# Kernel optimization log

Measured on AMD Instinct MI355X. Metric: run time of the kernel, lower is better.

The kernel has to match this reference:

```python
import jax, jax.numpy as jnp
import numpy as np

B, S, D, H = 2, 2048, 1024, 16
DK = D // H

def setup_inputs() -> dict:
    key = jax.random.key(0)
    ks = jax.random.split(key, 5)
    scale = 1.0 / np.sqrt(D)
    return {
        "query": jax.random.normal(ks[0], (B, S, D), dtype=jnp.float32),
        "mask": jnp.ones((B, S, S), dtype=jnp.int32),
        "Wq": jax.random.normal(ks[1], (D, D), dtype=jnp.float32) * scale,
        "bq": jnp.zeros((D,), dtype=jnp.float32),
        "Wk": jax.random.normal(ks[2], (D, D), dtype=jnp.float32) * scale,
        "bk": jnp.zeros((D,), dtype=jnp.float32),
        "Wv": jax.random.normal(ks[3], (D, D), dtype=jnp.float32) * scale,
        "bv": jnp.zeros((D,), dtype=jnp.float32),
        "Wo": jax.random.normal(ks[4], (D, D), dtype=jnp.float32) * scale,
        "bo": jnp.zeros((D,), dtype=jnp.float32),
    }

def reference(query, mask, Wq, bq, Wk, bk, Wv, bv, Wo, bo):
    # self-attention: key = value = query (torch Linear: x @ W.T + b)
    b, s, d = query.shape
    def proj(x, W, bias):
        y = jnp.einsum('bsd,ed->bse', x, W) + bias
        return y.reshape(b, s, H, DK).transpose(0, 2, 1, 3)  # [B,H,S,DK]
    q = proj(query, Wq, bq)
    k = proj(query, Wk, bk)
    v = proj(query, Wv, bv)
    scores = jnp.einsum('bhqd,bhkd->bhqk', q, k) / jnp.sqrt(jnp.float32(DK))
    m = mask[:, None, :, :]  # [B,1,S,S] (torch unsqueeze(1) for 3D mask)
    scores = jnp.where(m == 0, jnp.float32(-1e9), scores)
    w = jax.nn.softmax(scores, axis=-1)  # dropout: eval mode -> identity
    o = jnp.einsum('bhqk,bhkd->bhqd', w, v)
    o = o.transpose(0, 2, 1, 3).reshape(b, s, d)
    return jnp.einsum('bsd,ed->bse', o, Wo) + bo
```

## Files before the change

### kernel.cpp

```cpp
#include <hip/hip_runtime.h>


typedef _Float16 f16x8 __attribute__((ext_vector_type(8)));
typedef _Float16 f16x4 __attribute__((ext_vector_type(4)));
typedef _Float16 f16x2 __attribute__((ext_vector_type(2)));
typedef float    f32x4 __attribute__((ext_vector_type(4)));
typedef float    f32x16 __attribute__((ext_vector_type(16)));
typedef int      i32x4 __attribute__((ext_vector_type(4)));
typedef unsigned u32x2 __attribute__((ext_vector_type(2)));

#define MFMA32(a, b, c) __builtin_amdgcn_mfma_f32_32x32x16_f16(a, b, c, 0, 0, 0)
#define MFMA16(a, b, c) __builtin_amdgcn_mfma_f32_16x16x32_f16(a, b, c, 0, 0, 0)

#if __has_builtin(__builtin_amdgcn_exp2f)
#define EXP2(x) __builtin_amdgcn_exp2f(x)
#else
#define EXP2(x) exp2f(x)
#endif

__device__ __forceinline__ void gld16(const void* g, void* l) {
    __builtin_amdgcn_global_load_lds(
        (const __attribute__((address_space(1))) void*)g,
        (__attribute__((address_space(3))) void*)l, 16, 0, 0);
}

__device__ __forceinline__ void conv1k(const float* __restrict__ in,
                                       _Float16* __restrict__ out, int base) {
    const int i = base + threadIdx.x * 4;
    float4 v = *(const float4*)(in + i);
    f16x4 o;
    o.x = (_Float16)v.x; o.y = (_Float16)v.y; o.z = (_Float16)v.z; o.w = (_Float16)v.w;
    *(f16x4*)(out + i) = o;
}

__global__ void k_pre(const float* __restrict__ X, const float* __restrict__ Wq,
                      const float* __restrict__ Wk, const float* __restrict__ Wv,
                      const float* __restrict__ Wo,
                      _Float16* __restrict__ Xh, _Float16* __restrict__ Wqh,
                      _Float16* __restrict__ Wkh, _Float16* __restrict__ Wvh,
                      _Float16* __restrict__ Woh,
                      const int* __restrict__ mask, int* __restrict__ flag) {
    const int bid = blockIdx.x;
    if (bid < 4096)      conv1k(X,  Xh,  bid * 1024);
    else if (bid < 5120) conv1k(Wq, Wqh, (bid - 4096) * 1024);
    else if (bid < 6144) conv1k(Wk, Wkh, (bid - 5120) * 1024);
    else if (bid < 7168) conv1k(Wv, Wvh, (bid - 6144) * 1024);
    else if (bid < 8192) conv1k(Wo, Woh, (bid - 7168) * 1024);
    else {
        const int i = (bid - 8192) * 1024 + threadIdx.x * 4;
        int4 v = *(const int4*)(mask + i);
        if ((v.x == 0) | (v.y == 0) | (v.z == 0) | (v.w == 0)) atomicOr(flag, 1);
    }
}

__global__ __launch_bounds__(256, 3) void k_qkv(
    const _Float16* __restrict__ X,
    const _Float16* __restrict__ Wqh, const _Float16* __restrict__ Wkh,
    const _Float16* __restrict__ Wvh,
    const float* __restrict__ bq, const float* __restrict__ bk,
    const float* __restrict__ bv,
    _Float16* __restrict__ Qo, _Float16* __restrict__ Ko, _Float16* __restrict__ Vo)
{
    __shared__ _Float16 SH[128 * 136];
    _Float16* As = SH;
    _Float16* Bs = SH + 128 * 64;
    const int tid = threadIdx.x;
    const int lane = tid & 63, wv = tid >> 6;
    const int wrow = wv >> 1, wcol = wv & 1;
    const int l5 = lane & 31, half = lane >> 5;
    const int which = blockIdx.x >> 3;
    const _Float16* W   = which == 0 ? Wqh : which == 1 ? Wkh : Wvh;
    const float*   bias = which == 0 ? bq  : which == 1 ? bk  : bv;
    const int n0 = (blockIdx.x & 7) * 128;
    const int m0 = blockIdx.y * 128;

    f32x16 acc[2][2];
#pragma unroll
    for (int a = 0; a < 2; ++a)
#pragma unroll
        for (int bb = 0; bb < 2; ++bb)
#pragma unroll
            for (int r = 0; r < 16; ++r) acc[a][bb][r] = 0.f;

#pragma unroll 1
    for (int k0 = 0; k0 < 1024; k0 += 64) {
        __syncthreads();
#pragma unroll
        for (int it = 0; it < 4; ++it) {
            const int wbase = it * 256 + wv * 64;
            const int ci = wbase + lane;
            const int r = ci >> 3;
            const int c8 = (((ci & 7) ^ (r & 7)) * 8);
            gld16(X + (size_t)(m0 + r) * 1024 + k0 + c8, As + wbase * 8);
            gld16(W + (size_t)(n0 + r) * 1024 + k0 + c8, Bs + wbase * 8);
        }
        __syncthreads();
#pragma unroll
        for (int ks = 0; ks < 4; ++ks) {
            f16x8 af[2], bf[2];
#pragma unroll
            for (int mt = 0; mt < 2; ++mt)
                af[mt] = *(const f16x8*)(As + (wrow * 64 + mt * 32 + l5) * 64 +
                                         (((ks * 2 + half) ^ (l5 & 7)) * 8));
#pragma unroll
            for (int nt = 0; nt < 2; ++nt)
                bf[nt] = *(const f16x8*)(Bs + (wcol * 64 + nt * 32 + l5) * 64 +
                                         (((ks * 2 + half) ^ (l5 & 7)) * 8));
#pragma unroll
            for (int mt = 0; mt < 2; ++mt)
#pragma unroll
                for (int nt = 0; nt < 2; ++nt)
                    acc[mt][nt] = MFMA32(af[mt], bf[nt], acc[mt][nt]);
        }
    }

    __syncthreads();
    const int b_ = m0 >> 11;
    const int s_base = m0 & 2047;
    if (which == 2) {
#pragma unroll
        for (int nt = 0; nt < 2; ++nt) {
            const int e_l = wcol * 64 + nt * 32 + l5;
            const float bv_ = bias[n0 + e_l];
#pragma unroll
            for (int mt = 0; mt < 2; ++mt)
#pragma unroll
                for (int g = 0; g < 4; ++g) {
                    const int m_l = wrow * 64 + mt * 32 + 8 * g + 4 * half;
                    f16x4 pk;
#pragma unroll
                    for (int j = 0; j < 4; ++j)
                        pk[j] = (_Float16)(acc[mt][nt][4 * g + j] + bv_);
                    *(f16x4*)(SH + e_l * 136 + m_l) = pk;
                }
        }
        __syncthreads();
#pragma unroll
        for (int p = 0; p < 8; ++p) {
            const int e_l = p * 16 + (tid >> 4);
            const int s8 = (tid & 15) * 8;
            f16x8 vv = *(const f16x8*)(SH + e_l * 136 + s8);
            const int e = n0 + e_l;
            const int h = e >> 6, dk = e & 63;
            const int s0 = s_base + s8;
            const size_t idx = ((((size_t)(b_ * 16 + h) * 128 + (s0 >> 4)) * 2 +
                                (dk >> 5)) * 64 + (dk & 31) + 32 * ((s8 >> 3) & 1)) * 8;
            *(f16x8*)(Vo + idx) = vv;
        }
    } else {
        const float qs = (which == 0) ? 0.18033688011112042f : 1.0f;
#pragma unroll
        for (int nt = 0; nt < 2; ++nt) {
            const int e_l = wcol * 64 + nt * 32 + l5;
            const float bv_ = bias[n0 + e_l];
#pragma unroll
            for (int mt = 0; mt < 2; ++mt)
#pragma unroll
                for (int r = 0; r < 16; ++r) {
                    const int m_l = wrow * 64 + mt * 32 + (r & 3) + 8 * (r >> 2) + 4 * half;
                    SH[m_l * 136 + e_l] = (_Float16)((acc[mt][nt][r] + bv_) * qs);
                }
        }
        __syncthreads();
#pragma unroll
        for (int p = 0; p < 8; ++p) {
            const int m_l = p * 16 + (tid >> 4);
            const int c8 = (tid & 15) * 8;
            f16x8 vv = *(const f16x8*)(SH + m_l * 136 + c8);
            const int e = n0 + c8;
            const int h = e >> 6, dk = e & 63;
            const int s = s_base + m_l;
            if (which == 0) {
                *(f16x8*)(Qo + (((size_t)b_ * 16 + h) * 2048 + s) * 64 + dk) = vv;
            } else {
                const size_t idx = ((((size_t)(b_ * 16 + h) * 64 + (s >> 5)) * 4 +
                                    (dk >> 4)) * 64 + (s & 31) + 32 * ((dk >> 3) & 1)) * 8;
                *(f16x8*)(Ko + idx) = vv;
            }
        }
    }
}

__global__ __launch_bounds__(256, 4) void k_oproj(
    const _Float16* __restrict__ Oin, const _Float16* __restrict__ Woh,
    const float* __restrict__ bo, float* __restrict__ out)
{
    __shared__ _Float16 As[128 * 64];
    __shared__ _Float16 Bs[64 * 64];
    const int tid = threadIdx.x;
    const int lane = tid & 63, wv = tid >> 6;
    const int quad = lane >> 4, lc = lane & 15;
    const int n0 = blockIdx.x * 64;
    const int m0 = blockIdx.y * 128;

    const f32x4 fzero = {0.f, 0.f, 0.f, 0.f};
    f32x4 acc[2][4];
#pragma unroll
    for (int a = 0; a < 2; ++a)
#pragma unroll
        for (int bb = 0; bb < 4; ++bb) acc[a][bb] = fzero;

#pragma unroll 1
    for (int k0 = 0; k0 < 1024; k0 += 64) {
        __syncthreads();
#pragma unroll
        for (int it = 0; it < 4; ++it) {
            const int ci = it * 256 + tid;
            const int r = ci >> 3;
            const int c8 = (((ci & 7) ^ (r & 7)) * 8);
            gld16(Oin + (size_t)(m0 + r) * 1024 + k0 + c8, As + ci * 8);
        }
#pragma unroll
        for (int it = 0; it < 2; ++it) {
            const int ci = it * 256 + tid;
            const int r = ci >> 3;
            const int c8 = (((ci & 7) ^ (r & 7)) * 8);
            gld16(Woh + (size_t)(n0 + r) * 1024 + k0 + c8, Bs + ci * 8);
        }
        __syncthreads();
#pragma unroll
        for (int ks = 0; ks < 2; ++ks) {
            f16x8 af[2], bf[4];
#pragma unroll
            for (int mt = 0; mt < 2; ++mt)
                af[mt] = *(const f16x8*)(As + (wv * 32 + mt * 16 + lc) * 64 +
                                         (((ks * 4 + quad) ^ (lc & 7)) * 8));
#pragma unroll
            for (int nt = 0; nt < 4; ++nt)
                bf[nt] = *(const f16x8*)(Bs + (nt * 16 + lc) * 64 +
                                         (((ks * 4 + quad) ^ (lc & 7)) * 8));
#pragma unroll
            for (int mt = 0; mt < 2; ++mt)
#pragma unroll
                for (int nt = 0; nt < 4; ++nt)
                    acc[mt][nt] = MFMA16(af[mt], bf[nt], acc[mt][nt]);
        }
    }
#pragma unroll
    for (int nt = 0; nt < 4; ++nt) {
        const int e = n0 + nt * 16 + lc;
        const float bv_ = bo[e];
#pragma unroll
        for (int mt = 0; mt < 2; ++mt)
#pragma unroll
            for (int i = 0; i < 4; ++i) {
                const int m = m0 + wv * 32 + mt * 16 + quad * 4 + i;
                out[(size_t)m * 1024 + e] = acc[mt][nt][i] + bv_;
            }
    }
}

__global__ __launch_bounds__(256, 4) void k_attn(
    const _Float16* __restrict__ Q, const _Float16* __restrict__ Kp,
    const _Float16* __restrict__ Vp, const int* __restrict__ mask,
    const int* __restrict__ flag, _Float16* __restrict__ O)
{
    __shared__ float Os[2][32 * 64];
    __shared__ float Ls[2][32];

    const int tid = threadIdx.x;
    const int lane = tid & 63, wv = tid >> 6;
    const int l5 = lane & 31, half = lane >> 5;
    const int qt = wv >> 1, kh = wv & 1;
    const int bh = blockIdx.x;
    const int b = bh >> 4, h = bh & 15;
    const int qb = blockIdx.y * 64 + qt * 32;

    const _Float16* Qb = Q  + (size_t)bh * 2048 * 64;
    const _Float16* Kb = Kp + (size_t)bh * 131072;
    const _Float16* Vb = Vp + (size_t)bh * 131072;

    f16x8 qf[4];
#pragma unroll
    for (int kk = 0; kk < 4; ++kk)
        qf[kk] = *(const f16x8*)(Qb + (size_t)(qb + l5) * 64 + kk * 16 + half * 8);

    const f32x16 fz = {0.f, 0.f, 0.f, 0.f, 0.f, 0.f, 0.f, 0.f,
                       0.f, 0.f, 0.f, 0.f, 0.f, 0.f, 0.f, 0.f};
    const f16x2 one2 = {(_Float16)1.f, (_Float16)1.f};

    f32x16 o[2];
#pragma unroll
    for (int nt = 0; nt < 2; ++nt)
#pragma unroll
        for (int r = 0; r < 16; ++r) o[nt][r] = 0.f;
    float l_i = 0.f;

    const bool has_zero = (*flag != 0);

#pragma unroll 2
    for (int it = 0; it < 32; ++it) {
        const int kb = kh * 32 + it;
        f16x8 kf[4];
#pragma unroll
        for (int kk = 0; kk < 4; ++kk)
            kf[kk] = *(const f16x8*)(Kb + ((size_t)(kb * 4 + kk) * 64 + lane) * 8);
        f16x8 vf[4];
#pragma unroll
        for (int ks = 0; ks < 2; ++ks)
#pragma unroll
            for (int nt = 0; nt < 2; ++nt)
                vf[ks * 2 + nt] = *(const f16x8*)(Vb +
                    ((size_t)((kb * 2 + ks) * 2 + nt) * 64 + lane) * 8);

        __builtin_amdgcn_s_setprio(1);
        f32x16 st = MFMA32(kf[0], qf[0], fz);
        st = MFMA32(kf[1], qf[1], st);
        st = MFMA32(kf[2], qf[2], st);
        st = MFMA32(kf[3], qf[3], st);
        __builtin_amdgcn_s_setprio(0);

        if (has_zero) {
            const int q = qb + l5;
            const int* mr = mask + ((size_t)b * 2048 + q) * 2048 + kb * 32;
            for (int r = 0; r < 16; ++r) {
                const int kk_ = (r & 3) + 8 * (r >> 2) + 4 * half;
                if (mr[kk_] == 0) st[r] = -1e30f;
            }
        }

        unsigned u[8];
        float rs = 0.f;
#pragma unroll
        for (int j = 0; j < 8; ++j) {
            const float p0 = EXP2(st[2 * j]);
            const float p1 = EXP2(st[2 * j + 1]);
            u[j] = __builtin_bit_cast(unsigned, __builtin_amdgcn_cvt_pkrtz(p0, p1));
#if __has_builtin(__builtin_amdgcn_fdot2)
            rs = __builtin_amdgcn_fdot2(__builtin_bit_cast(f16x2, u[j]), one2, rs, false);
#else
            rs += p0 + p1;
#endif
        }
        rs += __shfl_xor(rs, 32);
        l_i += rs;

        u32x2 r02 = __builtin_amdgcn_permlane32_swap(u[0], u[2], false, false);
        u32x2 r13 = __builtin_amdgcn_permlane32_swap(u[1], u[3], false, false);
        u32x2 r46 = __builtin_amdgcn_permlane32_swap(u[4], u[6], false, false);
        u32x2 r57 = __builtin_amdgcn_permlane32_swap(u[5], u[7], false, false);
        i32x4 a0 = { (int)r02[0], (int)r13[0], (int)r02[1], (int)r13[1] };
        i32x4 a1 = { (int)r46[0], (int)r57[0], (int)r46[1], (int)r57[1] };
        f16x8 pa0 = __builtin_bit_cast(f16x8, a0);
        f16x8 pa1 = __builtin_bit_cast(f16x8, a1);

        __builtin_amdgcn_s_setprio(1);
        o[0] = MFMA32(pa0, vf[0], o[0]);
        o[1] = MFMA32(pa0, vf[1], o[1]);
        o[0] = MFMA32(pa1, vf[2], o[0]);
        o[1] = MFMA32(pa1, vf[3], o[1]);
        __builtin_amdgcn_s_setprio(0);
    }

    if (kh == 1) {
        if (half == 0) Ls[qt][l5] = l_i;
#pragma unroll
        for (int nt = 0; nt < 2; ++nt)
#pragma unroll
            for (int r = 0; r < 16; ++r) {
                const int q_loc = (r & 3) + 8 * (r >> 2) + 4 * half;
                Os[qt][q_loc * 64 + nt * 32 + l5] = o[nt][r];
            }
    }
    __syncthreads();
    if (kh == 0) {
        const float linv = 1.f / (l_i + Ls[qt][l5]);
#pragma unroll
        for (int r = 0; r < 16; ++r) {
            const int q_loc = (r & 3) + 8 * (r >> 2) + 4 * half;
            const float lv = __shfl(linv, q_loc);
            const int q = qb + q_loc;
            _Float16* orow = O + ((size_t)b * 2048 + q) * 1024 + h * 64;
#pragma unroll
            for (int nt = 0; nt < 2; ++nt) {
                const float val = o[nt][r] + Os[qt][q_loc * 64 + nt * 32 + l5];
                orow[nt * 32 + l5] = (_Float16)(val * lv);
            }
        }
    }
}

extern "C" void kernel_launch(void* const* d_in, const int* in_sizes, int n_in,
                              void* d_out, int out_size, void* d_ws, size_t ws_size,
                              hipStream_t stream) {
    const float* query = (const float*)d_in[0];
    const int*   mask  = (const int*)d_in[1];
    const float* Wq = (const float*)d_in[2]; const float* bq = (const float*)d_in[3];
    const float* Wk = (const float*)d_in[4]; const float* bk = (const float*)d_in[5];
    const float* Wv = (const float*)d_in[6]; const float* bv = (const float*)d_in[7];
    const float* Wo = (const float*)d_in[8]; const float* bo = (const float*)d_in[9];
    float* out = (float*)d_out;

    char* ws = (char*)d_ws;
    _Float16* Xh  = (_Float16*)(ws);
    _Float16* Wqh = (_Float16*)(ws + 8388608);
    _Float16* Wkh = (_Float16*)(ws + 10485760);
    _Float16* Wvh = (_Float16*)(ws + 12582912);
    _Float16* Woh = (_Float16*)(ws + 14680064);
    _Float16* Qh  = (_Float16*)(ws + 16777216);
    _Float16* Kh  = (_Float16*)(ws + 25165824);
    _Float16* Vh  = (_Float16*)(ws + 33554432);
    _Float16* Oh  = Xh;
    int* flag     = (int*)(ws + 41943040);

    (void)hipMemsetAsync(flag, 0, 4, stream);
    k_pre<<<16384, 256, 0, stream>>>(query, Wq, Wk, Wv, Wo,
                                     Xh, Wqh, Wkh, Wvh, Woh, mask, flag);
    k_qkv<<<dim3(24, 32), 256, 0, stream>>>(Xh, Wqh, Wkh, Wvh, bq, bk, bv, Qh, Kh, Vh);
    k_attn<<<dim3(32, 32), 256, 0, stream>>>(Qh, Kh, Vh, mask, flag, Oh);
    k_oproj<<<dim3(16, 32), 256, 0, stream>>>(Oh, Woh, bo, out);
}
```

Measured before the change: 214.4 us.

## Stage K/V tiles in double-buffered LDS shared by four query waves

The attention kernel now has each block cover 128 queries, with four waves each owning 32 queries over the full key range. Previously waves split the keys in half and merged partial outputs through shared memory. K and V tiles are loaded once per block into a double-buffered LDS area with async global-to-LDS loads and then read by all four waves, so global K/V traffic per query drops. In exchange there is a block-wide barrier every iteration and half as many blocks are launched (512), which may lower occupancy and latency hiding.

```diff
diff --git a/kernel.cpp b/kernel.cpp
--- a/kernel.cpp
+++ b/kernel.cpp
@@ -255,28 +255,24 @@
     const _Float16* __restrict__ Vp, const int* __restrict__ mask,
     const int* __restrict__ flag, _Float16* __restrict__ O)
 {
-    __shared__ float Os[2][32 * 64];
-    __shared__ float Ls[2][32];
+    __shared__ _Float16 KV[2 * 4096];
 
     const int tid = threadIdx.x;
     const int lane = tid & 63, wv = tid >> 6;
     const int l5 = lane & 31, half = lane >> 5;
-    const int qt = wv >> 1, kh = wv & 1;
     const int bh = blockIdx.x;
     const int b = bh >> 4, h = bh & 15;
-    const int qb = blockIdx.y * 64 + qt * 32;
+    const int qb = blockIdx.y * 128 + wv * 32;
 
     const _Float16* Qb = Q  + (size_t)bh * 2048 * 64;
-    const _Float16* Kb = Kp + (size_t)bh * 131072;
-    const _Float16* Vb = Vp + (size_t)bh * 131072;
+    const _Float16* Kst = Kp + (size_t)bh * 131072 + tid * 8;
+    const _Float16* Vst = Vp + (size_t)bh * 131072 + tid * 8;
 
     f16x8 qf[4];
 #pragma unroll
     for (int kk = 0; kk < 4; ++kk)
         qf[kk] = *(const f16x8*)(Qb + (size_t)(qb + l5) * 64 + kk * 16 + half * 8);
 
-    const f32x16 fz = {0.f, 0.f, 0.f, 0.f, 0.f, 0.f, 0.f, 0.f,
-                       0.f, 0.f, 0.f, 0.f, 0.f, 0.f, 0.f, 0.f};
     const f16x2 one2 = {(_Float16)1.f, (_Float16)1.f};
 
     f32x16 o[2];
@@ -288,23 +284,32 @@
 
     const bool has_zero = (*flag != 0);
 
+    gld16(Kst, KV + tid * 8);
+    gld16(Vst, KV + 2048 + tid * 8);
+    __syncthreads();
+
 #pragma unroll 2
-    for (int it = 0; it < 32; ++it) {
-        const int kb = kh * 32 + it;
-        f16x8 kf[4];
+    for (int it = 0; it < 64; ++it) {
+        const int cur = (it & 1) * 4096;
+        if (it < 63) {
+            const int nxt = cur ^ 4096;
+            gld16(Kst + (it + 1) * 2048, KV + nxt + tid * 8);
+            gld16(Vst + (it + 1) * 2048, KV + nxt + 2048 + tid * 8);
+        }
+
+        f16x8 kf[4], vf[4];
 #pragma unroll
         for (int kk = 0; kk < 4; ++kk)
-            kf[kk] = *(const f16x8*)(Kb + ((size_t)(kb * 4 + kk) * 64 + lane) * 8);
-        f16x8 vf[4];
-#pragma unroll
-        for (int ks = 0; ks < 2; ++ks)
-#pragma unroll
-            for (int nt = 0; nt < 2; ++nt)
-                vf[ks * 2 + nt] = *(const f16x8*)(Vb +
-                    ((size_t)((kb * 2 + ks) * 2 + nt) * 64 + lane) * 8);
-
+            kf[kk] = *(const f16x8*)(KV + cur + (kk * 64 + lane) * 8);
+#pragma unroll
+        for (int j = 0; j < 4; ++j)
+            vf[j] = *(const f16x8*)(KV + cur + 2048 + (j * 64 + lane) * 8);
+
+        f32x16 st;
+#pragma unroll
+        for (int r = 0; r < 16; ++r) st[r] = 0.f;
         __builtin_amdgcn_s_setprio(1);
-        f32x16 st = MFMA32(kf[0], qf[0], fz);
+        st = MFMA32(kf[0], qf[0], st);
         st = MFMA32(kf[1], qf[1], st);
         st = MFMA32(kf[2], qf[2], st);
         st = MFMA32(kf[3], qf[3], st);
@@ -312,7 +317,7 @@
 
         if (has_zero) {
             const int q = qb + l5;
-            const int* mr = mask + ((size_t)b * 2048 + q) * 2048 + kb * 32;
+            const int* mr = mask + ((size_t)b * 2048 + q) * 2048 + it * 32;
             for (int r = 0; r < 16; ++r) {
                 const int kk_ = (r & 3) + 8 * (r >> 2) + 4 * half;
                 if (mr[kk_] == 0) st[r] = -1e30f;
@@ -350,33 +355,20 @@
         o[0] = MFMA32(pa1, vf[2], o[0]);
         o[1] = MFMA32(pa1, vf[3], o[1]);
         __builtin_amdgcn_s_setprio(0);
-    }
-
-    if (kh == 1) {
-        if (half == 0) Ls[qt][l5] = l_i;
+
+        __syncthreads();
+    }
+
+    const float linv = 1.f / l_i;
+#pragma unroll
+    for (int r = 0; r < 16; ++r) {
+        const int q_loc = (r & 3) + 8 * (r >> 2) + 4 * half;
+        const float lv = __shfl(linv, q_loc);
+        const int q = qb + q_loc;
+        _Float16* orow = O + ((size_t)b * 2048 + q) * 1024 + h * 64;
 #pragma unroll
         for (int nt = 0; nt < 2; ++nt)
-#pragma unroll
-            for (int r = 0; r < 16; ++r) {
-                const int q_loc = (r & 3) + 8 * (r >> 2) + 4 * half;
-                Os[qt][q_loc * 64 + nt * 32 + l5] = o[nt][r];
-            }
-    }
-    __syncthreads();
-    if (kh == 0) {
-        const float linv = 1.f / (l_i + Ls[qt][l5]);
-#pragma unroll
-        for (int r = 0; r < 16; ++r) {
-            const int q_loc = (r & 3) + 8 * (r >> 2) + 4 * half;
-            const float lv = __shfl(linv, q_loc);
-            const int q = qb + q_loc;
-            _Float16* orow = O + ((size_t)b * 2048 + q) * 1024 + h * 64;
-#pragma unroll
-            for (int nt = 0; nt < 2; ++nt) {
-                const float val = o[nt][r] + Os[qt][q_loc * 64 + nt * 32 + l5];
-                orow[nt * 32 + l5] = (_Float16)(val * lv);
-            }
-        }
+            orow[nt * 32 + l5] = (_Float16)(o[nt][r] * lv);
     }
 }
 
@@ -407,6 +399,6 @@
     k_pre<<<16384, 256, 0, stream>>>(query, Wq, Wk, Wv, Wo,
                                      Xh, Wqh, Wkh, Wvh, Woh, mask, flag);
     k_qkv<<<dim3(24, 32), 256, 0, stream>>>(Xh, Wqh, Wkh, Wvh, bq, bk, bv, Qh, Kh, Vh);
-    k_attn<<<dim3(32, 32), 256, 0, stream>>>(Qh, Kh, Vh, mask, flag, Oh);
+    k_attn<<<dim3(32, 16), 256, 0, stream>>>(Qh, Kh, Vh, mask, flag, Oh);
     k_oproj<<<dim3(16, 32), 256, 0, stream>>>(Oh, Woh, bo, out);
 }
```

Result: faster. 205.7 us (-4.1%).
